# Kernel optimization log

Hardware: AMD Instinct MI355X
Metric: run time of the kernel (lower is better)

Reference implementation:

```python
import jax, jax.numpy as jnp
import numpy as np

EMBED = 1024
HEADS = 16
HEAD_DIM = EMBED // HEADS


def setup_inputs() -> dict:
    key = jax.random.key(0)
    ks = jax.random.split(key, 9)
    s = 1.0 / np.sqrt(EMBED)
    x = jax.random.normal(ks[0], (2, 2048, EMBED), dtype=jnp.float32)
    Wq = jax.random.uniform(ks[1], (EMBED, EMBED), jnp.float32, -s, s)
    bq = jax.random.uniform(ks[2], (EMBED,), jnp.float32, -s, s)
    Wk = jax.random.uniform(ks[3], (EMBED, EMBED), jnp.float32, -s, s)
    bk = jax.random.uniform(ks[4], (EMBED,), jnp.float32, -s, s)
    Wv = jax.random.uniform(ks[5], (EMBED, EMBED), jnp.float32, -s, s)
    bv = jax.random.uniform(ks[6], (EMBED,), jnp.float32, -s, s)
    Wo = jax.random.uniform(ks[7], (EMBED, EMBED), jnp.float32, -s, s)
    bo = jax.random.uniform(ks[8], (EMBED,), jnp.float32, -s, s)
    return {"x": x, "Wq": Wq, "bq": bq, "Wk": Wk, "bk": bk,
            "Wv": Wv, "bv": bv, "Wo": Wo, "bo": bo}


def reference(x, Wq, bq, Wk, bk, Wv, bv, Wo, bo):
    B, S, E = x.shape
    H, D = HEADS, HEAD_DIM
    # QKV projections, split heads: [B,S,E] -> [B,H,S,D]
    def proj(W, b):
        return (x @ W + b).reshape(B, S, H, D).transpose(0, 2, 1, 3)
    q, k, v = proj(Wq, bq), proj(Wk, bk), proj(Wv, bv)
    scores = jnp.einsum('bhsd,bhtd->bhst', q, k) / jnp.sqrt(jnp.float32(D))
    attn = jax.nn.softmax(scores, axis=-1)
    out = jnp.einsum('bhst,bhtd->bhsd', attn, v)  # [B,H,S,D]
    out = out.transpose(0, 2, 1, 3).reshape(B, S, E)
    return out @ Wo + bo
```

## Files before the change

### kernel.cpp

```cpp
#include <hip/hip_runtime.h>
#include <cstddef>
#include <cstdint>

#define EMB 1024
#define NH 16
#define HD 64
#define SEQ 2048
#define BATCH 2
#define MROWS 4096
#define LOG2E 1.4426950408889634f

typedef unsigned short u16;
typedef __attribute__((ext_vector_type(8))) short short8;
typedef __attribute__((ext_vector_type(4))) float floatx4;
typedef __attribute__((ext_vector_type(16))) float floatx16;
typedef __attribute__((ext_vector_type(2))) float f32x2;

#define MFMA32(a,b,c) __builtin_amdgcn_mfma_f32_16x16x32_bf16((a),(b),(c),0,0,0)
#define MFMA3216(a,b,c) __builtin_amdgcn_mfma_f32_32x32x16_bf16((a),(b),(c),0,0,0)

__device__ __forceinline__ u16 f2bf(float f) {
    union { float f; uint32_t u; } v; v.f = f;
    return (u16)((v.u + 0x7fffu + ((v.u >> 16) & 1u)) >> 16);
}
__device__ __forceinline__ uint32_t pk2u(uint32_t a, uint32_t b) {
    return __builtin_amdgcn_perm(b, a, 0x07060302u);
}
__device__ __forceinline__ float lo_f(uint32_t u) {
    union { uint32_t u; float f; } v; v.u = u << 16; return v.f;
}
__device__ __forceinline__ float hi_f(uint32_t u) {
    union { uint32_t u; float f; } v; v.u = u & 0xffff0000u; return v.f;
}
__device__ __forceinline__ void plswap(uint32_t &a, uint32_t &b) {
    asm volatile("v_permlane32_swap_b32 %0, %1" : "+v"(a), "+v"(b));
}
typedef const __attribute__((address_space(1))) void* gptr_t;
typedef __attribute__((address_space(3))) void* lptr_t;
__device__ __forceinline__ void gl2lds16(const void* g, void* l) {
    __builtin_amdgcn_global_load_lds((gptr_t)g, (lptr_t)l, 16, 0, 0);
}

__global__ __launch_bounds__(256) void cvt_all_k(
    const float* __restrict__ x,
    const float* __restrict__ W0, const float* __restrict__ W1,
    const float* __restrict__ W2, const float* __restrict__ W3,
    u16* __restrict__ Wt4, u16* __restrict__ xh) {
    const int z = blockIdx.z;
    const int tid = threadIdx.x;
    if (z == 4) {
        const int nb = gridDim.x * gridDim.y;
        const int bid = blockIdx.y * gridDim.x + blockIdx.x;
        const int stride = nb * 256 * 8;
        for (int i = (bid * 256 + tid) * 8; i < MROWS * EMB; i += stride) {
            float4 a = *(const float4*)(x + i);
            float4 b = *(const float4*)(x + i + 4);
            alignas(16) u16 o[8] = {f2bf(a.x), f2bf(a.y), f2bf(a.z), f2bf(a.w),
                                    f2bf(b.x), f2bf(b.y), f2bf(b.z), f2bf(b.w)};
            *(uint4*)(xh + i) = *(const uint4*)o;
        }
        return;
    }
    const float* W = (z == 0) ? W0 : (z == 1) ? W1 : (z == 2) ? W2 : W3;
    const float scale = (z == 0) ? 0.125f * LOG2E : 1.0f;
    u16* dst = Wt4 + (size_t)z * 1048576;
    __shared__ float Lf[64][65];
    const int kt = blockIdx.y * 64, nt = blockIdx.x * 64;
    {
        const int r = tid >> 2, c4 = (tid & 3) * 16;
        const float* src = W + (size_t)(kt + r) * EMB + nt + c4;
        #pragma unroll
        for (int i = 0; i < 16; i += 4) {
            float4 v = *(const float4*)(src + i);
            Lf[r][c4 + i + 0] = v.x; Lf[r][c4 + i + 1] = v.y;
            Lf[r][c4 + i + 2] = v.z; Lf[r][c4 + i + 3] = v.w;
        }
    }
    __syncthreads();
    const int n = tid >> 2, k4 = (tid & 3) * 16;
    alignas(16) u16 hb[16];
    #pragma unroll
    for (int i = 0; i < 16; ++i) hb[i] = f2bf(Lf[k4 + i][n] * scale);
    const size_t o = (size_t)(nt + n) * EMB + kt + k4;
    *(uint4*)(dst + o) = *(const uint4*)hb;
    *(uint4*)(dst + o + 8) = *(const uint4*)(hb + 8);
}

__global__ __launch_bounds__(256) void gemm_qkv_k(
    const u16* __restrict__ xh, const u16* __restrict__ Wt4,
    const float* __restrict__ b0, const float* __restrict__ b1,
    const float* __restrict__ b2,
    u16* __restrict__ Q, u16* __restrict__ K, u16* __restrict__ V) {
    const int flat = blockIdx.x + 8 * blockIdx.y + 256 * blockIdx.z;
    const int xcd = flat & 7, i6 = flat >> 3;
    const int z = i6 >> 5, j = i6 & 31;
    const int cm = xcd & 3, cn = xcd >> 2;
    const int bm = (cm * 8 + (j >> 2)) * 128;
    const int bn = (cn * 4 + (j & 3)) * 128;

    const u16* Wt = Wt4 + (size_t)z * 1048576;
    const float* bias = (z == 0) ? b0 : (z == 1) ? b1 : b2;
    u16* out = (z == 0) ? Q : (z == 1) ? K : V;
    const float bscale = (z == 0) ? 0.125f * LOG2E : 1.0f;
    __shared__ alignas(16) u16 As[2][4096];
    __shared__ alignas(16) u16 Bs[2][4096];
    const int tid = threadIdx.x;
    const int lane = tid & 63, w = tid >> 6;
    const int l15 = lane & 15, quad = lane >> 4;
    const int wm = (w & 1) * 64, wn = (w >> 1) * 64;

    floatx4 acc[4][4];
    const floatx4 zf = {0.f, 0.f, 0.f, 0.f};
    #pragma unroll
    for (int mt = 0; mt < 4; ++mt)
        #pragma unroll
        for (int nt = 0; nt < 4; ++nt) acc[mt][nt] = zf;

    const int c0 = tid, c1 = tid + 256;
    const int r0 = c0 >> 2, p0 = c0 & 3, cc0 = (p0 - r0 - (r0 >> 2)) & 3;
    const int r1 = c1 >> 2, p1 = c1 & 3, cc1 = (p1 - r1 - (r1 >> 2)) & 3;
    const u16* ag0 = xh + (size_t)(bm + r0) * EMB + cc0 * 8;
    const u16* ag1 = xh + (size_t)(bm + r1) * EMB + cc1 * 8;
    const u16* bg0 = Wt + (size_t)(bn + r0) * EMB + cc0 * 8;
    const u16* bg1 = Wt + (size_t)(bn + r1) * EMB + cc1 * 8;

    #define QSTAGE(bf, kk) do { \
        gl2lds16(ag0 + (kk), &As[bf][c0 * 8]); gl2lds16(ag1 + (kk), &As[bf][c1 * 8]); \
        gl2lds16(bg0 + (kk), &Bs[bf][c0 * 8]); gl2lds16(bg1 + (kk), &Bs[bf][c1 * 8]); } while (0)

    QSTAGE(0, 0);
    __syncthreads();
    for (int kt = 0; kt < EMB; kt += 32) {
        const int cur = (kt >> 5) & 1;
        if (kt + 32 < EMB) QSTAGE(cur ^ 1, kt + 32);
        short8 af[4], bf[4];
        #pragma unroll
        for (int t = 0; t < 4; ++t) {
            const int ra = wm + t * 16 + l15;
            const int rb = wn + t * 16 + l15;
            af[t] = *(const short8*)&As[cur][ra * 32 + ((quad + ra + (ra >> 2)) & 3) * 8];
            bf[t] = *(const short8*)&Bs[cur][rb * 32 + ((quad + rb + (rb >> 2)) & 3) * 8];
        }
        __builtin_amdgcn_s_setprio(1);
        #pragma unroll
        for (int mt = 0; mt < 4; ++mt)
            #pragma unroll
            for (int nt = 0; nt < 4; ++nt)
                acc[mt][nt] = MFMA32(af[mt], bf[nt], acc[mt][nt]);
        __builtin_amdgcn_s_setprio(0);
        __syncthreads();
    }

    #pragma unroll
    for (int nt = 0; nt < 4; ++nt) {
        const int col = bn + wn + nt * 16 + l15;
        const float bv = bias[col] * bscale;
        #pragma unroll
        for (int mt = 0; mt < 4; ++mt) {
            const int row = bm + wm + mt * 16 + quad * 4;
            #pragma unroll
            for (int r = 0; r < 4; ++r)
                out[(size_t)(row + r) * EMB + col] = f2bf(acc[mt][nt][r] + bv);
        }
    }
}

__global__ __launch_bounds__(256) void gemm_o_k(
    const u16* __restrict__ Ag, const u16* __restrict__ Wt,
    const float* __restrict__ bias, float* __restrict__ out) {
    const int flat = blockIdx.x + 16 * blockIdx.y;
    const int xcd = flat & 7, i6 = flat >> 3;
    const int cm = xcd & 3, cn = xcd >> 2;
    const int bm = (cm * 8 + (i6 >> 3)) * 128;
    const int bn = (cn * 8 + (i6 & 7)) * 64;
    __shared__ alignas(16) u16 As[2][4096];
    __shared__ alignas(16) u16 Bs[2][2048];
    const int tid = threadIdx.x;
    const int lane = tid & 63, w = tid >> 6;
    const int l15 = lane & 15, quad = lane >> 4;
    const int wm = w * 32;

    floatx4 acc[2][4];
    const floatx4 zf = {0.f, 0.f, 0.f, 0.f};
    #pragma unroll
    for (int mt = 0; mt < 2; ++mt)
        #pragma unroll
        for (int nt = 0; nt < 4; ++nt) acc[mt][nt] = zf;

    const int c0 = tid, c1 = tid + 256;
    const int r0 = c0 >> 2, p0 = c0 & 3, cc0 = (p0 - r0 - (r0 >> 2)) & 3;
    const int r1 = c1 >> 2, p1 = c1 & 3, cc1 = (p1 - r1 - (r1 >> 2)) & 3;
    const u16* ag0 = Ag + (size_t)(bm + r0) * EMB + cc0 * 8;
    const u16* ag1 = Ag + (size_t)(bm + r1) * EMB + cc1 * 8;
    const u16* bg0 = Wt + (size_t)(bn + r0) * EMB + cc0 * 8;

    #define OSTAGE(bf, kk) do { \
        gl2lds16(ag0 + (kk), &As[bf][c0 * 8]); \
        gl2lds16(ag1 + (kk), &As[bf][c1 * 8]); \
        if (c0 < 256) gl2lds16(bg0 + (kk), &Bs[bf][c0 * 8]); } while (0)

    OSTAGE(0, 0);
    __syncthreads();
    for (int kt = 0; kt < EMB; kt += 32) {
        const int cur = (kt >> 5) & 1;
        if (kt + 32 < EMB) OSTAGE(cur ^ 1, kt + 32);
        short8 af[2], bf[4];
        #pragma unroll
        for (int t = 0; t < 2; ++t) {
            const int ra = wm + t * 16 + l15;
            af[t] = *(const short8*)&As[cur][ra * 32 + ((quad + ra + (ra >> 2)) & 3) * 8];
        }
        #pragma unroll
        for (int t = 0; t < 4; ++t) {
            const int rb = t * 16 + l15;
            bf[t] = *(const short8*)&Bs[cur][rb * 32 + ((quad + rb + (rb >> 2)) & 3) * 8];
        }
        __builtin_amdgcn_s_setprio(1);
        #pragma unroll
        for (int mt = 0; mt < 2; ++mt)
            #pragma unroll
            for (int nt = 0; nt < 4; ++nt)
                acc[mt][nt] = MFMA32(af[mt], bf[nt], acc[mt][nt]);
        __builtin_amdgcn_s_setprio(0);
        __syncthreads();
    }

    #pragma unroll
    for (int nt = 0; nt < 4; ++nt) {
        const int col = bn + nt * 16 + l15;
        const float bv = bias[col];
        #pragma unroll
        for (int mt = 0; mt < 2; ++mt) {
            const int row = bm + wm + mt * 16 + quad * 4;
            #pragma unroll
            for (int r = 0; r < 4; ++r)
                out[(size_t)(row + r) * EMB + col] = acc[mt][nt][r] + bv;
        }
    }
}

__global__ __launch_bounds__(256) void vtrans_k(const u16* __restrict__ V,
                                                u16* __restrict__ Vt) {
    const int tt = blockIdx.x, h = blockIdx.y, b = blockIdx.z;
    __shared__ u16 Lt[64][72];
    const int tid = threadIdx.x;
    {
        const int r = tid >> 2, c4 = (tid & 3) * 16;
        const u16* src = V + (size_t)(b * SEQ + tt * 64 + r) * EMB + h * HD + c4;
        alignas(16) u16 buf[16];
        *(uint4*)buf = *(const uint4*)src;
        *(uint4*)(buf + 8) = *(const uint4*)(src + 8);
        #pragma unroll
        for (int i = 0; i < 16; ++i) Lt[c4 + i][r] = buf[i];
    }
    __syncthreads();
    const int d = tid >> 2, t4 = (tid & 3) * 16;
    u16* dst = Vt + ((size_t)((b * NH + h) * HD + d)) * SEQ + tt * 64 + t4;
    *(uint4*)dst = *(const uint4*)&Lt[d][t4];
    *(uint4*)(dst + 8) = *(const uint4*)&Lt[d][t4 + 8];
}

__global__ __launch_bounds__(256) void flash_k(
    const u16* __restrict__ Q, const u16* __restrict__ K,
    const u16* __restrict__ Vt,
    u16* __restrict__ Np0, u16* __restrict__ Np1,
    u16* __restrict__ Np2, u16* __restrict__ Np3,
    float* __restrict__ Lp) {
    const int flat = blockIdx.x + 16 * blockIdx.y + 256 * blockIdx.z;
    const int xcd = flat & 7, idx = flat >> 3;
    const int gid = xcd * 16 + (idx >> 4);
    const int qt = idx & 15;
    const int h = gid & 15, zz = gid >> 4;
    const int b = zz >> 2, sp = zz & 3;
    const int t0 = sp * (SEQ / 4);
    __shared__ alignas(16) u16 Ks[2][4096];
    __shared__ alignas(16) u16 Vs[2][4096];
    const int tid = threadIdx.x;
    const int lane = tid & 63, w = tid >> 6;
    const int l31 = lane & 31, hf = lane >> 5;

    const u16* qp = Q + (size_t)(b * SEQ + qt * 128 + w * 32 + l31) * EMB
                    + h * HD + hf * 8;
    short8 qb[4];
    #pragma unroll
    for (int c = 0; c < 4; ++c) qb[c] = *(const short8*)(qp + c * 16);

    const floatx16 z16 = {0.f, 0.f, 0.f, 0.f, 0.f, 0.f, 0.f, 0.f,
                          0.f, 0.f, 0.f, 0.f, 0.f, 0.f, 0.f, 0.f};
    floatx16 oacc[2];
    oacc[0] = z16; oacc[1] = z16;
    floatx16 lacc = z16;
    const short8 ones8 = {0x3F80, 0x3F80, 0x3F80, 0x3F80,
                          0x3F80, 0x3F80, 0x3F80, 0x3F80};

    const int s0 = tid, s1 = tid + 256;
    const int kr0 = s0 >> 3, kc0 = ((s0 & 7) - kr0) & 7;
    const int kr1 = s1 >> 3, kc1 = ((s1 & 7) - kr1) & 7;
    const u16* kg0 = K + (size_t)(b * SEQ + t0 + kr0) * EMB + h * HD + kc0 * 8;
    const u16* kg1 = K + (size_t)(b * SEQ + t0 + kr1) * EMB + h * HD + kc1 * 8;
    const u16* vg0 = Vt + ((size_t)((b * NH + h) * HD + kr0)) * SEQ + t0 + kc0 * 8;
    const u16* vg1 = Vt + ((size_t)((b * NH + h) * HD + kr1)) * SEQ + t0 + kc1 * 8;

    #define FSTAGE(bf, kk) do { \
        gl2lds16(kg0 + (size_t)(kk) * 64 * EMB, &Ks[bf][s0 * 8]); \
        gl2lds16(kg1 + (size_t)(kk) * 64 * EMB, &Ks[bf][s1 * 8]); \
        gl2lds16(vg0 + (kk) * 64, &Vs[bf][s0 * 8]); \
        gl2lds16(vg1 + (kk) * 64, &Vs[bf][s1 * 8]); } while (0)

    const int NT = SEQ / 4 / 64;
    FSTAGE(0, 0);
    __syncthreads();
    for (int kt = 0; kt < NT; ++kt) {
        const int cur = kt & 1;
        if (kt + 1 < NT) FSTAGE(cur ^ 1, kt + 1);

        short8 pa[4];
        #pragma unroll
        for (int tt = 0; tt < 2; ++tt) {
            floatx16 st = z16;
            const int r = tt * 32 + l31;
            __builtin_amdgcn_s_setprio(1);
            #pragma unroll
            for (int c = 0; c < 4; ++c) {
                const int jc = c * 2 + hf;
                const short8 ka = *(const short8*)&Ks[cur][r * 64 + ((jc + r) & 7) * 8];
                st = MFMA3216(ka, qb[c], st);
            }
            __builtin_amdgcn_s_setprio(0);
            uint32_t e[16];
            #pragma unroll
            for (int i = 0; i < 16; i += 2) {
                f32x2 v = {st[i], st[i + 1]};
                v = v * 8388608.0f + 1064992512.0f;
                e[i] = (uint32_t)(int)v.x;
                e[i + 1] = (uint32_t)(int)v.y;
            }
            #pragma unroll
            for (int c = 0; c < 2; ++c) {
                uint32_t w0 = pk2u(e[c * 8 + 0], e[c * 8 + 1]);
                uint32_t w1 = pk2u(e[c * 8 + 2], e[c * 8 + 3]);
                uint32_t w2 = pk2u(e[c * 8 + 4], e[c * 8 + 5]);
                uint32_t w3 = pk2u(e[c * 8 + 6], e[c * 8 + 7]);
                plswap(w0, w2);
                plswap(w1, w3);
                union { uint32_t uu[4]; short8 s; } pk_;
                pk_.uu[0] = w0; pk_.uu[1] = w1; pk_.uu[2] = w2; pk_.uu[3] = w3;
                pa[tt * 2 + c] = pk_.s;
            }
        }

        __builtin_amdgcn_s_setprio(1);
        #pragma unroll
        for (int dt = 0; dt < 2; ++dt) {
            const int vr = dt * 32 + l31;
            #pragma unroll
            for (int g = 0; g < 4; ++g) {
                const int jc = g * 2 + hf;
                const short8 vb = *(const short8*)&Vs[cur][vr * 64 + ((jc + vr) & 7) * 8];
                oacc[dt] = MFMA3216(pa[g], vb, oacc[dt]);
            }
        }
        #pragma unroll
        for (int g = 0; g < 4; ++g) lacc = MFMA3216(pa[g], ones8, lacc);
        __builtin_amdgcn_s_setprio(0);

        __syncthreads();
    }

    u16* np = (sp == 0) ? Np0 : (sp == 1) ? Np1 : (sp == 2) ? Np2 : Np3;
    float* lp = Lp + (size_t)sp * (MROWS * NH);

    if (l31 == 0) {
        #pragma unroll
        for (int r = 0; r < 16; ++r) {
            const int qloc = (r & 3) + 8 * (r >> 2) + 4 * hf;
            const int qrow = qt * 128 + w * 32 + qloc;
            lp[(size_t)(b * SEQ + qrow) * NH + h] = lacc[r];
        }
    }

    #pragma unroll
    for (int dt = 0; dt < 2; ++dt)
        #pragma unroll
        for (int r = 0; r < 16; ++r) {
            const int qloc = (r & 3) + 8 * (r >> 2) + 4 * hf;
            const size_t o =
                (size_t)(b * SEQ + qt * 128 + w * 32 + qloc) * EMB
                + h * HD + dt * 32 + l31;
            np[o] = f2bf(oacc[dt][r]);
        }
}

__global__ __launch_bounds__(256) void reduce_k(
    const u16* __restrict__ Np0, const u16* __restrict__ Np1,
    const u16* __restrict__ Np2, const u16* __restrict__ Np3,
    const float* __restrict__ Lp, u16* __restrict__ AO) {
    const int i = blockIdx.x * 256 + threadIdx.x;
    const int e = i * 4;
    const int row = e >> 10;
    const int hh = (e & 1023) >> 6;
    const size_t lx = (size_t)row * NH + hh;
    const float lsum = Lp[lx] + Lp[(size_t)(MROWS * NH) + lx] +
                       Lp[2 * (size_t)(MROWS * NH) + lx] +
                       Lp[3 * (size_t)(MROWS * NH) + lx];
    const float inv = 1.f / lsum;
    const uint2 n0 = *(const uint2*)(Np0 + e);
    const uint2 n1 = *(const uint2*)(Np1 + e);
    const uint2 n2 = *(const uint2*)(Np2 + e);
    const uint2 n3 = *(const uint2*)(Np3 + e);
    const float x0 = (lo_f(n0.x) + lo_f(n1.x) + lo_f(n2.x) + lo_f(n3.x)) * inv;
    const float x1 = (hi_f(n0.x) + hi_f(n1.x) + hi_f(n2.x) + hi_f(n3.x)) * inv;
    const float x2 = (lo_f(n0.y) + lo_f(n1.y) + lo_f(n2.y) + lo_f(n3.y)) * inv;
    const float x3 = (hi_f(n0.y) + hi_f(n1.y) + hi_f(n2.y) + hi_f(n3.y)) * inv;
    uint2 o;
    o.x = (uint32_t)f2bf(x0) | ((uint32_t)f2bf(x1) << 16);
    o.y = (uint32_t)f2bf(x2) | ((uint32_t)f2bf(x3) << 16);
    *(uint2*)(AO + e) = o;
}

extern "C" void kernel_launch(void* const* d_in, const int* in_sizes, int n_in,
                              void* d_out, int out_size, void* d_ws, size_t ws_size,
                              hipStream_t stream) {
    const float* x  = (const float*)d_in[0];
    const float* Wq = (const float*)d_in[1];
    const float* bq = (const float*)d_in[2];
    const float* Wk = (const float*)d_in[3];
    const float* bk = (const float*)d_in[4];
    const float* Wv = (const float*)d_in[5];
    const float* bv = (const float*)d_in[6];
    const float* Wo = (const float*)d_in[7];
    const float* bo = (const float*)d_in[8];

    u16* ws16 = (u16*)d_ws;
    const size_t P4 = (size_t)MROWS * EMB;
    u16* xh  = ws16;
    u16* Qb  = ws16 + P4;
    u16* Kb  = ws16 + 2 * P4;
    u16* Vb  = ws16 + 3 * P4;
    u16* Vtb = ws16 + 4 * P4;
    u16* Wt4 = ws16 + 5 * P4;
    u16* N2  = ws16 + 6 * P4;
    u16* N3  = ws16 + 7 * P4;
    float* Lp = (float*)(ws16 + 8 * P4);

    cvt_all_k<<<dim3(16, 16, 5), 256, 0, stream>>>(x, Wq, Wk, Wv, Wo, Wt4, xh);
    gemm_qkv_k<<<dim3(8, 32, 3), 256, 0, stream>>>(xh, Wt4, bq, bk, bv, Qb, Kb, Vb);
    vtrans_k<<<dim3(32, 16, 2), 256, 0, stream>>>(Vb, Vtb);
    flash_k<<<dim3(16, 16, 8), 256, 0, stream>>>(Qb, Kb, Vtb, xh, Vb, N2, N3, Lp);
    reduce_k<<<4096, 256, 0, stream>>>(xh, Vb, N2, N3, Lp, Qb);
    gemm_o_k<<<dim3(16, 32, 1), 256, 0, stream>>>(Qb, Wt4 + 3 * 1048576, bo, (float*)d_out);
}
```

Baseline: 203.2 us.

## Fuse split-K attention partial reduction into output projection GEMM A-tile loading

Removes the separate reduce_k kernel and instead has gemm_o_k load the four partial attention outputs plus the log-sum partials, combine and normalize them in registers, and write the bf16 A tile into LDS. This saves one launch and a write and reread of the combined attention output. The cost is that each GEMM tile now reads four times as much A data through plain global loads instead of direct global-to-LDS loads. Because gemm_o_k uses 16 column blocks, every A tile is reduced 16 times over, which adds redundant memory traffic and ALU work inside the GEMM main loop.

After: 238.3 us. 1.17x slower.

```diff
diff --git a/kernel.cpp b/kernel.cpp
--- a/kernel.cpp
+++ b/kernel.cpp
@@ -39,6 +39,12 @@
 typedef __attribute__((address_space(3))) void* lptr_t;
 __device__ __forceinline__ void gl2lds16(const void* g, void* l) {
     __builtin_amdgcn_global_load_lds((gptr_t)g, (lptr_t)l, 16, 0, 0);
+}
+__device__ __forceinline__ uint32_t fuse2(uint32_t w0, uint32_t w1, uint32_t w2,
+                                          uint32_t w3, float inv) {
+    const float lo = (((lo_f(w0) + lo_f(w1)) + lo_f(w2)) + lo_f(w3)) * inv;
+    const float hi = (((hi_f(w0) + hi_f(w1)) + hi_f(w2)) + hi_f(w3)) * inv;
+    return (uint32_t)f2bf(lo) | ((uint32_t)f2bf(hi) << 16);
 }
 
 __global__ __launch_bounds__(256) void cvt_all_k(
@@ -166,7 +172,10 @@
 }
 
 __global__ __launch_bounds__(256) void gemm_o_k(
-    const u16* __restrict__ Ag, const u16* __restrict__ Wt,
+    const u16* __restrict__ Np0, const u16* __restrict__ Np1,
+    const u16* __restrict__ Np2, const u16* __restrict__ Np3,
+    const float* __restrict__ Lp,
+    const u16* __restrict__ Wt,
     const float* __restrict__ bias, float* __restrict__ out) {
     const int flat = blockIdx.x + 16 * blockIdx.y;
     const int xcd = flat & 7, i6 = flat >> 3;
@@ -179,6 +188,7 @@
     const int lane = tid & 63, w = tid >> 6;
     const int l15 = lane & 15, quad = lane >> 4;
     const int wm = w * 32;
+    const int PL = MROWS * NH;
 
     floatx4 acc[2][4];
     const floatx4 zf = {0.f, 0.f, 0.f, 0.f};
@@ -190,20 +200,54 @@
     const int c0 = tid, c1 = tid + 256;
     const int r0 = c0 >> 2, p0 = c0 & 3, cc0 = (p0 - r0 - (r0 >> 2)) & 3;
     const int r1 = c1 >> 2, p1 = c1 & 3, cc1 = (p1 - r1 - (r1 >> 2)) & 3;
-    const u16* ag0 = Ag + (size_t)(bm + r0) * EMB + cc0 * 8;
-    const u16* ag1 = Ag + (size_t)(bm + r1) * EMB + cc1 * 8;
+    const size_t ga0 = (size_t)(bm + r0) * EMB + cc0 * 8;
+    const size_t ga1 = (size_t)(bm + r1) * EMB + cc1 * 8;
+    const size_t lx0 = (size_t)(bm + r0) * NH;
+    const size_t lx1 = (size_t)(bm + r1) * NH;
     const u16* bg0 = Wt + (size_t)(bn + r0) * EMB + cc0 * 8;
 
-    #define OSTAGE(bf, kk) do { \
-        gl2lds16(ag0 + (kk), &As[bf][c0 * 8]); \
-        gl2lds16(ag1 + (kk), &As[bf][c1 * 8]); \
+    uint4 s0n0, s0n1, s0n2, s0n3, s1n0, s1n1, s1n2, s1n3;
+    float inv0, inv1;
+
+    #define OLOADA(kk) do { \
+        s0n0 = *(const uint4*)(Np0 + ga0 + (kk)); \
+        s0n1 = *(const uint4*)(Np1 + ga0 + (kk)); \
+        s0n2 = *(const uint4*)(Np2 + ga0 + (kk)); \
+        s0n3 = *(const uint4*)(Np3 + ga0 + (kk)); \
+        s1n0 = *(const uint4*)(Np0 + ga1 + (kk)); \
+        s1n1 = *(const uint4*)(Np1 + ga1 + (kk)); \
+        s1n2 = *(const uint4*)(Np2 + ga1 + (kk)); \
+        s1n3 = *(const uint4*)(Np3 + ga1 + (kk)); \
+        const int hh_ = (kk) >> 6; \
+        const float l0_ = ((Lp[lx0 + hh_] + Lp[PL + lx0 + hh_]) + \
+                           Lp[2 * PL + lx0 + hh_]) + Lp[3 * PL + lx0 + hh_]; \
+        const float l1_ = ((Lp[lx1 + hh_] + Lp[PL + lx1 + hh_]) + \
+                           Lp[2 * PL + lx1 + hh_]) + Lp[3 * PL + lx1 + hh_]; \
+        inv0 = 1.f / l0_; inv1 = 1.f / l1_; } while (0)
+
+    #define OPROC(bf) do { \
+        uint4 o0, o1; \
+        o0.x = fuse2(s0n0.x, s0n1.x, s0n2.x, s0n3.x, inv0); \
+        o0.y = fuse2(s0n0.y, s0n1.y, s0n2.y, s0n3.y, inv0); \
+        o0.z = fuse2(s0n0.z, s0n1.z, s0n2.z, s0n3.z, inv0); \
+        o0.w = fuse2(s0n0.w, s0n1.w, s0n2.w, s0n3.w, inv0); \
+        o1.x = fuse2(s1n0.x, s1n1.x, s1n2.x, s1n3.x, inv1); \
+        o1.y = fuse2(s1n0.y, s1n1.y, s1n2.y, s1n3.y, inv1); \
+        o1.z = fuse2(s1n0.z, s1n1.z, s1n2.z, s1n3.z, inv1); \
+        o1.w = fuse2(s1n0.w, s1n1.w, s1n2.w, s1n3.w, inv1); \
+        *((uint4*)&As[bf][c0 * 8]) = o0; \
+        *((uint4*)&As[bf][c1 * 8]) = o1; } while (0)
+
+    #define OSTAGEB(bf, kk) do { \
         if (c0 < 256) gl2lds16(bg0 + (kk), &Bs[bf][c0 * 8]); } while (0)
 
-    OSTAGE(0, 0);
+    OLOADA(0); OSTAGEB(0, 0);
+    OPROC(0);
     __syncthreads();
     for (int kt = 0; kt < EMB; kt += 32) {
         const int cur = (kt >> 5) & 1;
-        if (kt + 32 < EMB) OSTAGE(cur ^ 1, kt + 32);
+        const bool more = (kt + 32 < EMB);
+        if (more) { OLOADA(kt + 32); OSTAGEB(cur ^ 1, kt + 32); }
         short8 af[2], bf[4];
         #pragma unroll
         for (int t = 0; t < 2; ++t) {
@@ -222,6 +266,7 @@
             for (int nt = 0; nt < 4; ++nt)
                 acc[mt][nt] = MFMA32(af[mt], bf[nt], acc[mt][nt]);
         __builtin_amdgcn_s_setprio(0);
+        if (more) OPROC(cur ^ 1);
         __syncthreads();
     }
 
@@ -391,33 +436,6 @@
         }
 }
 
-__global__ __launch_bounds__(256) void reduce_k(
-    const u16* __restrict__ Np0, const u16* __restrict__ Np1,
-    const u16* __restrict__ Np2, const u16* __restrict__ Np3,
-    const float* __restrict__ Lp, u16* __restrict__ AO) {
-    const int i = blockIdx.x * 256 + threadIdx.x;
-    const int e = i * 4;
-    const int row = e >> 10;
-    const int hh = (e & 1023) >> 6;
-    const size_t lx = (size_t)row * NH + hh;
-    const float lsum = Lp[lx] + Lp[(size_t)(MROWS * NH) + lx] +
-                       Lp[2 * (size_t)(MROWS * NH) + lx] +
-                       Lp[3 * (size_t)(MROWS * NH) + lx];
-    const float inv = 1.f / lsum;
-    const uint2 n0 = *(const uint2*)(Np0 + e);
-    const uint2 n1 = *(const uint2*)(Np1 + e);
-    const uint2 n2 = *(const uint2*)(Np2 + e);
-    const uint2 n3 = *(const uint2*)(Np3 + e);
-    const float x0 = (lo_f(n0.x) + lo_f(n1.x) + lo_f(n2.x) + lo_f(n3.x)) * inv;
-    const float x1 = (hi_f(n0.x) + hi_f(n1.x) + hi_f(n2.x) + hi_f(n3.x)) * inv;
-    const float x2 = (lo_f(n0.y) + lo_f(n1.y) + lo_f(n2.y) + lo_f(n3.y)) * inv;
-    const float x3 = (hi_f(n0.y) + hi_f(n1.y) + hi_f(n2.y) + hi_f(n3.y)) * inv;
-    uint2 o;
-    o.x = (uint32_t)f2bf(x0) | ((uint32_t)f2bf(x1) << 16);
-    o.y = (uint32_t)f2bf(x2) | ((uint32_t)f2bf(x3) << 16);
-    *(uint2*)(AO + e) = o;
-}
-
 extern "C" void kernel_launch(void* const* d_in, const int* in_sizes, int n_in,
                               void* d_out, int out_size, void* d_ws, size_t ws_size,
                               hipStream_t stream) {
@@ -447,6 +465,7 @@
     gemm_qkv_k<<<dim3(8, 32, 3), 256, 0, stream>>>(xh, Wt4, bq, bk, bv, Qb, Kb, Vb);
     vtrans_k<<<dim3(32, 16, 2), 256, 0, stream>>>(Vb, Vtb);
     flash_k<<<dim3(16, 16, 8), 256, 0, stream>>>(Qb, Kb, Vtb, xh, Vb, N2, N3, Lp);
-    reduce_k<<<4096, 256, 0, stream>>>(xh, Vb, N2, N3, Lp, Qb);
-    gemm_o_k<<<dim3(16, 32, 1), 256, 0, stream>>>(Qb, Wt4 + 3 * 1048576, bo, (float*)d_out);
-}
+    gemm_o_k<<<dim3(16, 32, 1), 256, 0, stream>>>(xh, Vb, N2, N3, Lp,
+                                                  Wt4 + 3 * 1048576, bo,
+                                                  (float*)d_out);
+}
```

## Fuse V transpose into QKV GEMM epilogue and single-buffer flash K/V tiles

Applied to the files above, without the earlier changes.

The QKV GEMM now writes V directly in the transposed per-head layout [b,h,d,s] using 4-element packed stores, so the separate vtrans kernel and its extra read/write pass over V are removed. Separately, the flash kernel drops its double-buffered K/V shared-memory staging in favour of a single buffer loaded with syncs around each tile. That halves LDS use and may raise occupancy, but it serializes loads with compute and loses prefetch overlap. The transposed V stores are strided, with 8-byte writes per lane, which may coalesce poorly.

Result: slower. 212.4 us (+4.5%).

```diff
diff --git a/kernel.cpp b/kernel.cpp
--- a/kernel.cpp
+++ b/kernel.cpp
@@ -90,7 +90,7 @@
     const u16* __restrict__ xh, const u16* __restrict__ Wt4,
     const float* __restrict__ b0, const float* __restrict__ b1,
     const float* __restrict__ b2,
-    u16* __restrict__ Q, u16* __restrict__ K, u16* __restrict__ V) {
+    u16* __restrict__ Q, u16* __restrict__ K, u16* __restrict__ Vt) {
     const int flat = blockIdx.x + 8 * blockIdx.y + 256 * blockIdx.z;
     const int xcd = flat & 7, i6 = flat >> 3;
     const int z = i6 >> 5, j = i6 & 31;
@@ -100,7 +100,7 @@
 
     const u16* Wt = Wt4 + (size_t)z * 1048576;
     const float* bias = (z == 0) ? b0 : (z == 1) ? b1 : b2;
-    u16* out = (z == 0) ? Q : (z == 1) ? K : V;
+    u16* out = (z == 0) ? Q : (z == 1) ? K : Vt;
     const float bscale = (z == 0) ? 0.125f * LOG2E : 1.0f;
     __shared__ alignas(16) u16 As[2][4096];
     __shared__ alignas(16) u16 Bs[2][4096];
@@ -151,16 +151,35 @@
         __syncthreads();
     }
 
-    #pragma unroll
-    for (int nt = 0; nt < 4; ++nt) {
-        const int col = bn + wn + nt * 16 + l15;
-        const float bv = bias[col] * bscale;
-        #pragma unroll
-        for (int mt = 0; mt < 4; ++mt) {
-            const int row = bm + wm + mt * 16 + quad * 4;
-            #pragma unroll
-            for (int r = 0; r < 4; ++r)
-                out[(size_t)(row + r) * EMB + col] = f2bf(acc[mt][nt][r] + bv);
+    if (z == 2) {
+        #pragma unroll
+        for (int nt = 0; nt < 4; ++nt) {
+            const int col = bn + wn + nt * 16 + l15;
+            const int hh = col >> 6, d = col & 63;
+            const float bv = bias[col] * bscale;
+            #pragma unroll
+            for (int mt = 0; mt < 4; ++mt) {
+                const int row = bm + wm + mt * 16 + quad * 4;
+                const int bb = row >> 11, s = row & 2047;
+                alignas(8) u16 o4[4];
+                #pragma unroll
+                for (int r = 0; r < 4; ++r) o4[r] = f2bf(acc[mt][nt][r] + bv);
+                *(uint2*)(out + ((size_t)((bb * NH + hh) * HD + d)) * SEQ + s) =
+                    *(const uint2*)o4;
+            }
+        }
+    } else {
+        #pragma unroll
+        for (int nt = 0; nt < 4; ++nt) {
+            const int col = bn + wn + nt * 16 + l15;
+            const float bv = bias[col] * bscale;
+            #pragma unroll
+            for (int mt = 0; mt < 4; ++mt) {
+                const int row = bm + wm + mt * 16 + quad * 4;
+                #pragma unroll
+                for (int r = 0; r < 4; ++r)
+                    out[(size_t)(row + r) * EMB + col] = f2bf(acc[mt][nt][r] + bv);
+            }
         }
     }
 }
@@ -239,27 +258,6 @@
     }
 }
 
-__global__ __launch_bounds__(256) void vtrans_k(const u16* __restrict__ V,
-                                                u16* __restrict__ Vt) {
-    const int tt = blockIdx.x, h = blockIdx.y, b = blockIdx.z;
-    __shared__ u16 Lt[64][72];
-    const int tid = threadIdx.x;
-    {
-        const int r = tid >> 2, c4 = (tid & 3) * 16;
-        const u16* src = V + (size_t)(b * SEQ + tt * 64 + r) * EMB + h * HD + c4;
-        alignas(16) u16 buf[16];
-        *(uint4*)buf = *(const uint4*)src;
-        *(uint4*)(buf + 8) = *(const uint4*)(src + 8);
-        #pragma unroll
-        for (int i = 0; i < 16; ++i) Lt[c4 + i][r] = buf[i];
-    }
-    __syncthreads();
-    const int d = tid >> 2, t4 = (tid & 3) * 16;
-    u16* dst = Vt + ((size_t)((b * NH + h) * HD + d)) * SEQ + tt * 64 + t4;
-    *(uint4*)dst = *(const uint4*)&Lt[d][t4];
-    *(uint4*)(dst + 8) = *(const uint4*)&Lt[d][t4 + 8];
-}
-
 __global__ __launch_bounds__(256) void flash_k(
     const u16* __restrict__ Q, const u16* __restrict__ K,
     const u16* __restrict__ Vt,
@@ -273,8 +271,8 @@
     const int h = gid & 15, zz = gid >> 4;
     const int b = zz >> 2, sp = zz & 3;
     const int t0 = sp * (SEQ / 4);
-    __shared__ alignas(16) u16 Ks[2][4096];
-    __shared__ alignas(16) u16 Vs[2][4096];
+    __shared__ alignas(16) u16 Ks[4096];
+    __shared__ alignas(16) u16 Vs[4096];
     const int tid = threadIdx.x;
     const int lane = tid & 63, w = tid >> 6;
     const int l31 = lane & 31, hf = lane >> 5;
@@ -301,18 +299,17 @@
     const u16* vg0 = Vt + ((size_t)((b * NH + h) * HD + kr0)) * SEQ + t0 + kc0 * 8;
     const u16* vg1 = Vt + ((size_t)((b * NH + h) * HD + kr1)) * SEQ + t0 + kc1 * 8;
 
-    #define FSTAGE(bf, kk) do { \
-        gl2lds16(kg0 + (size_t)(kk) * 64 * EMB, &Ks[bf][s0 * 8]); \
-        gl2lds16(kg1 + (size_t)(kk) * 64 * EMB, &Ks[bf][s1 * 8]); \
-        gl2lds16(vg0 + (kk) * 64, &Vs[bf][s0 * 8]); \
-        gl2lds16(vg1 + (kk) * 64, &Vs[bf][s1 * 8]); } while (0)
+    #define FSTAGE(kk) do { \
+        gl2lds16(kg0 + (size_t)(kk) * 64 * EMB, &Ks[s0 * 8]); \
+        gl2lds16(kg1 + (size_t)(kk) * 64 * EMB, &Ks[s1 * 8]); \
+        gl2lds16(vg0 + (kk) * 64, &Vs[s0 * 8]); \
+        gl2lds16(vg1 + (kk) * 64, &Vs[s1 * 8]); } while (0)
 
     const int NT = SEQ / 4 / 64;
-    FSTAGE(0, 0);
-    __syncthreads();
     for (int kt = 0; kt < NT; ++kt) {
-        const int cur = kt & 1;
-        if (kt + 1 < NT) FSTAGE(cur ^ 1, kt + 1);
+        __syncthreads();
+        FSTAGE(kt);
+        __syncthreads();
 
         short8 pa[4];
         #pragma unroll
@@ -323,7 +320,7 @@
             #pragma unroll
             for (int c = 0; c < 4; ++c) {
                 const int jc = c * 2 + hf;
-                const short8 ka = *(const short8*)&Ks[cur][r * 64 + ((jc + r) & 7) * 8];
+                const short8 ka = *(const short8*)&Ks[r * 64 + ((jc + r) & 7) * 8];
                 st = MFMA3216(ka, qb[c], st);
             }
             __builtin_amdgcn_s_setprio(0);
@@ -356,15 +353,13 @@
             #pragma unroll
             for (int g = 0; g < 4; ++g) {
                 const int jc = g * 2 + hf;
-                const short8 vb = *(const short8*)&Vs[cur][vr * 64 + ((jc + vr) & 7) * 8];
+                const short8 vb = *(const short8*)&Vs[vr * 64 + ((jc + vr) & 7) * 8];
                 oacc[dt] = MFMA3216(pa[g], vb, oacc[dt]);
             }
         }
         #pragma unroll
         for (int g = 0; g < 4; ++g) lacc = MFMA3216(pa[g], ones8, lacc);
         __builtin_amdgcn_s_setprio(0);
-
-        __syncthreads();
     }
 
     u16* np = (sp == 0) ? Np0 : (sp == 1) ? Np1 : (sp == 2) ? Np2 : Np3;
@@ -444,8 +439,7 @@
     float* Lp = (float*)(ws16 + 8 * P4);
 
     cvt_all_k<<<dim3(16, 16, 5), 256, 0, stream>>>(x, Wq, Wk, Wv, Wo, Wt4, xh);
-    gemm_qkv_k<<<dim3(8, 32, 3), 256, 0, stream>>>(xh, Wt4, bq, bk, bv, Qb, Kb, Vb);
-    vtrans_k<<<dim3(32, 16, 2), 256, 0, stream>>>(Vb, Vtb);
+    gemm_qkv_k<<<dim3(8, 32, 3), 256, 0, stream>>>(xh, Wt4, bq, bk, bv, Qb, Kb, Vtb);
     flash_k<<<dim3(16, 16, 8), 256, 0, stream>>>(Qb, Kb, Vtb, xh, Vb, N2, N3, Lp);
     reduce_k<<<4096, 256, 0, stream>>>(xh, Vb, N2, N3, Lp, Qb);
     gemm_o_k<<<dim3(16, 32, 1), 256, 0, stream>>>(Qb, Wt4 + 3 * 1048576, bo, (float*)d_out);
```
